# Kernel optimization log

Hardware: AMD Instinct MI355X
Metric: run time of the kernel (lower is better)

## Reference

```python
import jax, jax.numpy as jnp
import numpy as np

V, E, H, B, T = 32000, 256, 512, 64, 24

def setup_inputs() -> dict:
    key = jax.random.key(0)
    ks = jax.random.split(key, 24)
    def n(k, shape, s=0.02):
        return jax.random.normal(k, shape, dtype=jnp.float32) * s
    inp = {
        "question_feat": n(ks[0], (B, H), 1.0),
        "image_feat": n(ks[1], (B, H), 1.0),
        "answer_seq": jax.random.randint(ks[2], (B, T), 0, V),
        "embedding": n(ks[3], (V, E)),
        "attn_W": n(ks[4], (H, 3 * H)),
        "attn_b": jnp.zeros((H,), jnp.float32),
        "v_W": n(ks[5], (1, H)),
        "fc_W": n(ks[6], (V, H)),
        "fc_b": jnp.zeros((V,), jnp.float32),
    }
    in_sizes = [E + 2 * H, H, H]  # layer0 sees cat(embed, context)=1280
    for l in range(3):
        inp[f"W_ih{l}"] = n(ks[7 + 4 * l], (4 * H, in_sizes[l]))
        inp[f"W_hh{l}"] = n(ks[8 + 4 * l], (4 * H, H))
        inp[f"b_ih{l}"] = jnp.zeros((4 * H,), jnp.float32)
        inp[f"b_hh{l}"] = jnp.zeros((4 * H,), jnp.float32)
    return inp

def _lstm_cell(x, h, c, W_ih, W_hh, b_ih, b_hh):
    # torch gate order: i, f, g, o
    g = x @ W_ih.T + b_ih + h @ W_hh.T + b_hh
    i, f, gg, o = jnp.split(g, 4, axis=-1)
    c_new = jax.nn.sigmoid(f) * c + jax.nn.sigmoid(i) * jnp.tanh(gg)
    h_new = jax.nn.sigmoid(o) * jnp.tanh(c_new)
    return h_new, c_new

def reference(question_feat, image_feat, answer_seq, embedding, attn_W, attn_b, v_W,
              fc_W, fc_b,
              W_ih0, W_hh0, b_ih0, b_hh0,
              W_ih1, W_hh1, b_ih1, b_hh1,
              W_ih2, W_hh2, b_ih2, b_hh2):
    combined = jnp.concatenate([question_feat, image_feat], axis=1)  # [B, 2H]
    x = embedding[answer_seq]            # [B, T, E]
    xs = jnp.swapaxes(x, 0, 1)           # [T, B, E]
    Ws = ((W_ih0, W_hh0, b_ih0, b_hh0),
          (W_ih1, W_hh1, b_ih1, b_hh1),
          (W_ih2, W_hh2, b_ih2, b_hh2))

    def step(carry, x_t):
        h, c, prev_attn = carry          # h, c: [3, B, H]; prev_attn: [B, H]
        energy = jnp.tanh(jnp.concatenate([prev_attn, combined], axis=1) @ attn_W.T + attn_b)
        aw = jax.nn.softmax(energy @ v_W.T, axis=1)  # [B, 1] (softmax over singleton, faithful to source)
        ctx = aw * combined                          # [B, 2H]
        cur = jnp.concatenate([x_t, ctx], axis=1)    # [B, E+2H]
        hs, cs = [], []
        for l in range(3):
            nh, nc = _lstm_cell(cur, h[l], c[l], *Ws[l])
            hs.append(nh); cs.append(nc); cur = nh
        logits = cur @ fc_W.T + fc_b                 # [B, V]
        return (jnp.stack(hs), jnp.stack(cs), cur), logits

    hdim = question_feat.shape[1]
    bsz = question_feat.shape[0]
    h0 = jnp.zeros((3, bsz, hdim), question_feat.dtype)
    c0 = jnp.zeros((3, bsz, hdim), question_feat.dtype)
    _, outs = jax.lax.scan(step, (h0, c0, question_feat), xs)
    return jnp.swapaxes(outs, 0, 1)  # [B, T, V]
```

## Files before the change

### kernel.cpp

```cpp
#include <hip/hip_runtime.h>
#include <hip/hip_bf16.h>
#include <stdint.h>


typedef short bf16x8 __attribute__((ext_vector_type(8)));
typedef float f32x4 __attribute__((ext_vector_type(4)));

#define NLSTM 96
#define FCB   160
#define NTILE_N 250
#define HSLOT 32768

__device__ __forceinline__ unsigned short f2b(float f) {
    uint32_t u = __builtin_bit_cast(uint32_t, f);
    uint32_t r = u + 0x7FFFu + ((u >> 16) & 1u);
    return (unsigned short)(r >> 16);
}
__device__ __forceinline__ float fsig(float x) {
    float e = __expf(-x);
    return __builtin_amdgcn_rcpf(1.0f + e);
}
__device__ __forceinline__ float ftanh(float x) {
    float e = __expf(-2.0f * x);
    return (1.0f - e) * __builtin_amdgcn_rcpf(1.0f + e);
}

__global__ __launch_bounds__(128) void pack_w(
    const float* __restrict__ Whh0,
    const float* __restrict__ Wih1, const float* __restrict__ Whh1,
    const float* __restrict__ Wih2, const float* __restrict__ Whh2,
    unsigned short* __restrict__ Wpk)
{
    int gid = blockIdx.x;
    int layer = gid / (32 * 64);
    int rem = gid % (32 * 64);
    int lbid = rem >> 6, r = rem & 63;
    int q = r >> 4, jj = r & 15;
    int grow = q * 512 + lbid * 16 + jj;
    int K = (layer == 0) ? 512 : 1024;
    size_t wbase = (layer == 0) ? 0
                 : (layer == 1) ? (size_t)32 * 64 * 512
                                : (size_t)32 * 64 * 512 + (size_t)32 * 64 * 1024;
    unsigned short* dst = Wpk + wbase + ((size_t)lbid * 64 + r) * K;
    const float *s0, *s1 = nullptr;
    if (layer == 0)      { s0 = Whh0 + (size_t)grow * 512; }
    else if (layer == 1) { s0 = Wih1 + (size_t)grow * 512; s1 = Whh1 + (size_t)grow * 512; }
    else                 { s0 = Wih2 + (size_t)grow * 512; s1 = Whh2 + (size_t)grow * 512; }
    {
        int k4 = threadIdx.x;
        f32x4 v = *(const f32x4*)&s0[k4 * 4];
        unsigned short o[4];
        #pragma unroll
        for (int j = 0; j < 4; ++j) o[j] = f2b(v[j]);
        *(uint64_t*)&dst[k4 * 4] = *(uint64_t*)o;
    }
    if (s1) {
        int k4 = threadIdx.x;
        f32x4 v = *(const f32x4*)&s1[k4 * 4];
        unsigned short o[4];
        #pragma unroll
        for (int j = 0; j < 4; ++j) o[j] = f2b(v[j]);
        *(uint64_t*)&dst[512 + k4 * 4] = *(uint64_t*)o;
    }
}

__global__ __launch_bounds__(256) void build_x(
    const float* __restrict__ qf,
    const float* __restrict__ imf,
    const int* __restrict__ seq,
    const float* __restrict__ emb,
    unsigned short* __restrict__ X)
{
    int r = blockIdx.x;
    int t = r >> 6, b = r & 63;
    int tok = seq[b * 24 + t];
    for (int e = threadIdx.x; e < 1280; e += 256) {
        float v;
        if (e < 256)      v = emb[(size_t)tok * 256 + e];
        else if (e < 768) v = qf[b * 512 + (e - 256)];
        else              v = imf[b * 512 + (e - 768)];
        X[(size_t)r * 1280 + e] = f2b(v);
    }
}

__global__ __launch_bounds__(256) void gemm128(
    const unsigned short* __restrict__ A, int lda,
    const float* __restrict__ Wf, int ldb,
    int K,
    const float* __restrict__ bias0,
    const float* __restrict__ bias1,
    float* __restrict__ outf, int ldo, int mblocks, int xcdq)
{
    __shared__ unsigned short lA[128 * 72];
    __shared__ unsigned short lB[128 * 72];
    int lin = blockIdx.x;
    int wg = (lin & 7) * xcdq + (lin >> 3);
    const int m0 = (wg % mblocks) * 128, n0 = (wg / mblocks) * 128;
    const int tid = threadIdx.x;
    const int lane = tid & 63, wid = tid >> 6;
    const int wm = wid >> 1, wn = wid & 1;

    f32x4 acc[4][4] = {};

    for (int kt = 0; kt < K; kt += 64) {
        #pragma unroll
        for (int c = 0; c < 4; ++c) {
            int chunk = tid + c * 256;
            int row = chunk >> 3, kc = (chunk & 7) * 8;
            *(bf16x8*)&lA[row * 72 + kc] =
                *(const bf16x8*)&A[(size_t)(m0 + row) * lda + kt + kc];
            const float* bp = &Wf[(size_t)(n0 + row) * ldb + kt + kc];
            f32x4 v0 = *(const f32x4*)bp;
            f32x4 v1 = *(const f32x4*)(bp + 4);
            unsigned short o[8];
            #pragma unroll
            for (int x = 0; x < 4; ++x) { o[x] = f2b(v0[x]); o[4 + x] = f2b(v1[x]); }
            *(bf16x8*)&lB[row * 72 + kc] = *(bf16x8*)o;
        }
        __syncthreads();
        #pragma unroll
        for (int ks = 0; ks < 64; ks += 32) {
            int kl = ks + ((lane >> 4) << 3);
            bf16x8 af[4], bfr[4];
            #pragma unroll
            for (int i = 0; i < 4; ++i)
                af[i] = *(const bf16x8*)&lA[(wm * 64 + i * 16 + (lane & 15)) * 72 + kl];
            #pragma unroll
            for (int j = 0; j < 4; ++j)
                bfr[j] = *(const bf16x8*)&lB[(wn * 64 + j * 16 + (lane & 15)) * 72 + kl];
            #pragma unroll
            for (int i = 0; i < 4; ++i)
                #pragma unroll
                for (int j = 0; j < 4; ++j)
                    acc[i][j] = __builtin_amdgcn_mfma_f32_16x16x32_bf16(
                        af[i], bfr[j], acc[i][j], 0, 0, 0);
        }
        __syncthreads();
    }

    #pragma unroll
    for (int i = 0; i < 4; ++i) {
        #pragma unroll
        for (int j = 0; j < 4; ++j) {
            int n = n0 + wn * 64 + j * 16 + (lane & 15);
            float bias = bias0[n] + bias1[n];
            #pragma unroll
            for (int r = 0; r < 4; ++r) {
                int m = m0 + wm * 64 + i * 16 + ((lane >> 4) << 2) + r;
                outf[(size_t)m * ldo + n] = acc[i][j][r] + bias;
            }
        }
    }
}

#define ISSUE_CHUNK(buf, kb0)                                                 \
    {                                                                         \
        _Pragma("unroll")                                                     \
        for (int u_ = 0; u_ < 8; ++u_) {                                      \
            int kg_ = (kb0) + u_ * 32 + lk;                                   \
            const unsigned short* hb_ = (kg_ < 512) ? A0 : A1;                \
            int kk_ = kg_ & 511;                                              \
            const unsigned short* ap_ =                                       \
                hb_ + ((kk_ >> 4) << 10) + brow16 + (kk_ & 15);               \
            asm volatile("global_load_dwordx4 %0, %1, off sc1"                \
                         : "=v"(buf[u_]) : "v"(ap_) : "memory");              \
        }                                                                     \
    }
#define MFMA_CHUNK(buf, kb0)                                                  \
    {                                                                         \
        _Pragma("unroll")                                                     \
        for (int u_ = 0; u_ < 8; ++u_) {                                      \
            int ksl_ = (kb0) + u_ * 32 + lk;                                  \
            _Pragma("unroll")                                                 \
            for (int q_ = 0; q_ < 4; ++q_) {                                  \
                int gx_ = ((ksl_ >> 3) ^ (lrow & 7)) << 3;                    \
                bf16x8 bq_ = *(const bf16x8*)&lb[(q_ * 16 + lrow) * K + gx_]; \
                acc[q_] = __builtin_amdgcn_mfma_f32_16x16x32_bf16(            \
                    buf[u_], bq_, acc[q_], 0, 0, 0);                          \
            }                                                                 \
        }                                                                     \
    }
#define VM_WAIT(n) { asm volatile("s_waitcnt vmcnt(" #n ")" ::: "memory");    \
                     __builtin_amdgcn_sched_barrier(0); }

#define FC_ISSUE_G(buf, ks0)                                                  \
    {                                                                         \
        _Pragma("unroll")                                                     \
        for (int u_ = 0; u_ < 4; ++u_) {                                      \
            _Pragma("unroll")                                                 \
            for (int i_ = 0; i_ < 4; ++i_) {                                  \
                int rm_ = m0 + wm * 64 + i_ * 16 + lrow;                      \
                int k_ = (ks0) + u_ * 32 + lk;                                \
                const unsigned short* ap_ = h2                                \
                    + (size_t)((rm_ >> 6) + 1) * HSLOT                        \
                    + ((k_ >> 4) << 10) + ((rm_ & 63) << 4) + (k_ & 15);      \
                asm volatile("global_load_dwordx4 %0, %1, off sc1"            \
                             : "=v"(buf[u_ * 4 + i_]) : "v"(ap_) : "memory"); \
            }                                                                 \
        }                                                                     \
    }
#define FC_MFMA_G(buf, ks0)                                                   \
    {                                                                         \
        _Pragma("unroll")                                                     \
        for (int u_ = 0; u_ < 4; ++u_) {                                      \
            int ks_ = (ks0) + u_ * 32 + lk;                                   \
            _Pragma("unroll")                                                 \
            for (int jj_ = 0; jj_ < 4; ++jj_) {                               \
                int row_ = wn * 64 + jj_ * 16 + lrow;                         \
                int gx_ = ((ks_ >> 3) ^ (row_ & 7)) << 3;                     \
                bf16x8 bq_ = *(const bf16x8*)&lB[row_ * 512 + gx_];           \
                _Pragma("unroll")                                             \
                for (int i_ = 0; i_ < 4; ++i_)                                \
                    acc[i_][jj_] = __builtin_amdgcn_mfma_f32_16x16x32_bf16(   \
                        buf[u_ * 4 + i_], bq_, acc[i_][jj_], 0, 0, 0);        \
            }                                                                 \
        }                                                                     \
    }

__global__ __launch_bounds__(256, 1) void fused_wave(
    const unsigned short* __restrict__ Wpk,
    const float* __restrict__ G0,
    const float* __restrict__ bih1, const float* __restrict__ bhh1,
    const float* __restrict__ bih2, const float* __restrict__ bhh2,
    unsigned short* __restrict__ hst,
    unsigned int* __restrict__ flags,
    const float* __restrict__ fcW,
    const float* __restrict__ fcb,
    float* __restrict__ out)
{
    extern __shared__ char smem[];
    const int bid = blockIdx.x;
    const int tid = threadIdx.x;
    const int lane = tid & 63, w = tid >> 6;
    const int lrow = lane & 15, lk = (lane >> 4) * 8;

    if (bid < NLSTM) {
        unsigned short* lb = (unsigned short*)smem;
        unsigned int* lcnt = (unsigned int*)(smem + 131072);
        const int layer = bid >> 5;
        const int lbid = bid & 31;
        const int j0 = lbid * 16;

        const int K = (layer == 0) ? 512 : 1024;
        const size_t wbase = (layer == 0) ? 0
                           : (layer == 1) ? (size_t)32 * 64 * 512
                                          : (size_t)32 * 64 * 512 + (size_t)32 * 64 * 1024;
        const unsigned short* Wblk = Wpk + wbase + (size_t)lbid * 64 * K;

        if (tid < 24) lcnt[tid] = 0;
        {
            const int kshift = (layer == 0) ? 6 : 7;
            const int gm = (K >> 3) - 1;
            const int total = 64 << kshift;
            for (int idx = tid; idx < total; idx += 256) {
                int row = idx >> kshift, g = idx & gm;
                int gx = g ^ (row & 7);
                *(bf16x8*)&lb[row * K + gx * 8] =
                    *(const bf16x8*)&Wblk[(size_t)row * K + g * 8];
            }
        }
        __syncthreads();

        unsigned short* hl = hst + (size_t)layer * 25 * HSLOT;
        const unsigned short* hlow =
            (layer > 0) ? hst + (size_t)(layer - 1) * 25 * HSLOT : nullptr;

        float pb[4] = {0.f, 0.f, 0.f, 0.f};
        if (layer == 1) {
            #pragma unroll
            for (int q = 0; q < 4; ++q)
                pb[q] = bih1[q * 512 + j0 + lrow] + bhh1[q * 512 + j0 + lrow];
        } else if (layer == 2) {
            #pragma unroll
            for (int q = 0; q < 4; ++q)
                pb[q] = bih2[q * 512 + j0 + lrow] + bhh2[q * 512 + j0 + lrow];
        }

        float creg[4] = {0.f, 0.f, 0.f, 0.f};
        const int brow16 = (w * 16 + lrow) << 4;

        for (int t = 0; t < 24; ++t) {
            float g0p[16];
            if (layer == 0) {
                const float* gp = G0 + (size_t)t * 64 * 2048;
                #pragma unroll
                for (int r = 0; r < 4; ++r) {
                    int b = w * 16 + ((lane >> 4) << 2) + r;
                    #pragma unroll
                    for (int q = 0; q < 4; ++q)
                        g0p[r * 4 + q] = gp[(size_t)b * 2048 + q * 512 + j0 + lrow];
                }
            }
            if (layer > 0 || t > 0) {
                const unsigned int* f1;
                const unsigned int* f2 = nullptr;
                if (layer == 0) {
                    f1 = flags + (t - 1) * 32;
                } else {
                    f1 = flags + ((layer - 1) * 24 + t) * 32;
                    if (t > 0) f2 = flags + (layer * 24 + t - 1) * 32;
                }
                const unsigned int* fp = (lane < 32) ? f1 : (f2 ? f2 : f1);
                int idx = lane & 31;
                while (true) {
                    unsigned v = __hip_atomic_load((unsigned int*)&fp[idx],
                                                   __ATOMIC_RELAXED,
                                                   __HIP_MEMORY_SCOPE_AGENT);
                    if (__all(v != 0)) break;
                    __builtin_amdgcn_s_sleep(2);
                }
            }

            const unsigned short* A0 = (layer == 0)
                ? hl + (size_t)t * HSLOT
                : hlow + (size_t)(t + 1) * HSLOT;
            const unsigned short* A1 = (layer == 0)
                ? A0
                : hl + (size_t)t * HSLOT;

            f32x4 acc[4] = {};
            bf16x8 bufA[8], bufB[8], bufC[8], bufD[8];
            if (K == 1024) {
                ISSUE_CHUNK(bufA, 0); ISSUE_CHUNK(bufB, 256);
                ISSUE_CHUNK(bufC, 512); ISSUE_CHUNK(bufD, 768);
                VM_WAIT(24); MFMA_CHUNK(bufA, 0);
                VM_WAIT(16); MFMA_CHUNK(bufB, 256);
                VM_WAIT(8);  MFMA_CHUNK(bufC, 512);
                VM_WAIT(0);  MFMA_CHUNK(bufD, 768);
            } else {
                ISSUE_CHUNK(bufA, 0); ISSUE_CHUNK(bufB, 256);
                VM_WAIT(8); MFMA_CHUNK(bufA, 0);
                VM_WAIT(0); MFMA_CHUNK(bufB, 256);
            }

            unsigned short* hslot = hl + (size_t)(t + 1) * HSLOT + (lbid << 10);
            #pragma unroll
            for (int r = 0; r < 4; ++r) {
                int b = w * 16 + ((lane >> 4) << 2) + r;
                float g[4];
                #pragma unroll
                for (int q = 0; q < 4; ++q) {
                    float p = (layer == 0) ? g0p[r * 4 + q] : pb[q];
                    g[q] = acc[q][r] + p;
                }
                float ig = fsig(g[0]);
                float fg = fsig(g[1]);
                float gg = ftanh(g[2]);
                float og = fsig(g[3]);
                float cn = fg * creg[r] + ig * gg;
                creg[r] = cn;
                float h = og * ftanh(cn);
                unsigned int hb = (unsigned int)f2b(h);
                unsigned short* hp = hslot + (b << 4) + lrow;
                asm volatile("global_store_short %0, %1, off sc1"
                             :: "v"(hp), "v"(hb) : "memory");
            }
            asm volatile("s_waitcnt vmcnt(0)" ::: "memory");
            if (lane == 0) {
                unsigned old = atomicAdd(&lcnt[t], 1u);
                if (old == 3u)
                    __hip_atomic_store(&flags[(layer * 24 + t) * 32 + lbid], 1u,
                                       __ATOMIC_RELAXED, __HIP_MEMORY_SCOPE_AGENT);
            }
        }
    } else {
        unsigned short* lB = (unsigned short*)smem;
        const int f = bid - NLSTM;
        const int wm = w >> 1, wn = w & 1;
        const unsigned short* h2 = hst + (size_t)2 * 25 * HSLOT;

        for (int p = 0; p < 2; ++p) {
            int ntp = f + p * FCB;
            if (ntp >= NTILE_N) break;
            int n0 = ntp * 128;
            __syncthreads();
            for (int idx = tid; idx < 128 * 64; idx += 256) {
                int row = idx >> 6, g = idx & 63;
                const float* bp = &fcW[(size_t)(n0 + row) * 512 + g * 8];
                f32x4 v0 = *(const f32x4*)bp;
                f32x4 v1 = *(const f32x4*)(bp + 4);
                unsigned short o[8];
                #pragma unroll
                for (int x = 0; x < 4; ++x) { o[x] = f2b(v0[x]); o[4 + x] = f2b(v1[x]); }
                *(bf16x8*)&lB[row * 512 + ((g ^ (row & 7)) << 3)] = *(bf16x8*)o;
            }
            __syncthreads();

            for (int mt = 0; mt < 12; ++mt) {
                if (tid < 64) {
                    const unsigned int* fb = flags + (2 * 24 + 2 * mt) * 32;
                    while (true) {
                        unsigned v = __hip_atomic_load((unsigned int*)&fb[lane],
                                                       __ATOMIC_RELAXED,
                                                       __HIP_MEMORY_SCOPE_AGENT);
                        if (__all(v != 0)) break;
                        __builtin_amdgcn_s_sleep(32);
                    }
                }
                __syncthreads();

                int m0 = mt * 128;
                f32x4 acc[4][4] = {};
                bf16x8 gA[16], gB[16];
                FC_ISSUE_G(gA, 0); FC_ISSUE_G(gB, 128);
                VM_WAIT(16); FC_MFMA_G(gA, 0);
                FC_ISSUE_G(gA, 256);
                VM_WAIT(16); FC_MFMA_G(gB, 128);
                FC_ISSUE_G(gB, 384);
                VM_WAIT(16); FC_MFMA_G(gA, 256);
                VM_WAIT(0);  FC_MFMA_G(gB, 384);

                #pragma unroll
                for (int i = 0; i < 4; ++i) {
                    #pragma unroll
                    for (int jj = 0; jj < 4; ++jj) {
                        int n = n0 + wn * 64 + jj * 16 + lrow;
                        float bias = fcb[n];
                        #pragma unroll
                        for (int r = 0; r < 4; ++r) {
                            int m = m0 + wm * 64 + i * 16 + ((lane >> 4) << 2) + r;
                            int b = m & 63, t = m >> 6;
                            __builtin_nontemporal_store(
                                acc[i][jj][r] + bias,
                                &out[(size_t)(b * 24 + t) * 32000 + n]);
                        }
                    }
                }
            }
        }
    }
}

extern "C" void kernel_launch(void* const* d_in, const int* in_sizes, int n_in,
                              void* d_out, int out_size, void* d_ws, size_t ws_size,
                              hipStream_t stream) {
    const float* qf  = (const float*)d_in[0];
    const float* imf = (const float*)d_in[1];
    const int*   seq = (const int*)d_in[2];
    const float* emb = (const float*)d_in[3];
    const float* fcW = (const float*)d_in[7];
    const float* fcb = (const float*)d_in[8];
    const float* Wih[3] = {(const float*)d_in[9],  (const float*)d_in[13], (const float*)d_in[17]};
    const float* Whh[3] = {(const float*)d_in[10], (const float*)d_in[14], (const float*)d_in[18]};
    const float* bih[3] = {(const float*)d_in[11], (const float*)d_in[15], (const float*)d_in[19]};
    const float* bhh[3] = {(const float*)d_in[12], (const float*)d_in[16], (const float*)d_in[20]};

    char* ws = (char*)d_ws;
    unsigned short* X     = (unsigned short*)(ws + 0);
    float*          G0    = (float*)(ws + 3932160);
    unsigned short* hst   = (unsigned short*)(ws + 16515072);
    unsigned int*   flags = (unsigned int*)(ws + 21430272);
    unsigned short* Wpk   = (unsigned short*)(ws + 21440000);

    hipMemsetAsync(flags, 0, 9216, stream);
    for (int l = 0; l < 3; ++l)
        hipMemsetAsync(hst + (size_t)l * 25 * HSLOT, 0, HSLOT * 2, stream);

    pack_w<<<3 * 32 * 64, 128, 0, stream>>>(Whh[0], Wih[1], Whh[1], Wih[2], Whh[2], Wpk);
    build_x<<<1536, 256, 0, stream>>>(qf, imf, seq, emb, X);

    gemm128<<<192, 256, 0, stream>>>(
        X, 1280, Wih[0], 1280, 1280, bih[0], bhh[0], G0, 2048, 12, 192 / 8);

    fused_wave<<<NLSTM + FCB, 256, 131200, stream>>>(
        Wpk, G0, bih[1], bhh[1], bih[2], bhh[2], hst, flags,
        fcW, fcb, (float*)d_out);
}
```

Measured before the change: 317.0 us.

## Use per-wave completion flags and stage FC A-tiles through LDS

LSTM blocks no longer count completed waves with an LDS atomic before setting one flag per block. Each wave now sets its own flag, and consumers poll four times as many flags, which removes the intra-block counter serialization. The FC blocks now load the h-state A tiles into a 16 KB LDS buffer with global_load_lds in 8 k-chunks, then do MFMA from LDS. This replaces the direct global-to-register double-buffered loads. The change adds more syncthreads, drops the register-level load/compute overlap, and enlarges the flag area and the LDS allocation.

```diff
diff --git a/kernel.cpp b/kernel.cpp
--- a/kernel.cpp
+++ b/kernel.cpp
@@ -23,6 +23,11 @@
 __device__ __forceinline__ float ftanh(float x) {
     float e = __expf(-2.0f * x);
     return (1.0f - e) * __builtin_amdgcn_rcpf(1.0f + e);
+}
+__device__ __forceinline__ void gload_lds16(const unsigned short* g, unsigned short* l) {
+    __builtin_amdgcn_global_load_lds(
+        (const __attribute__((address_space(1))) unsigned int*)g,
+        (__attribute__((address_space(3))) unsigned int*)l, 16, 0, 16);
 }
 
 __global__ __launch_bounds__(128) void pack_w(
@@ -183,40 +188,6 @@
 #define VM_WAIT(n) { asm volatile("s_waitcnt vmcnt(" #n ")" ::: "memory");    \
                      __builtin_amdgcn_sched_barrier(0); }
 
-#define FC_ISSUE_G(buf, ks0)                                                  \
-    {                                                                         \
-        _Pragma("unroll")                                                     \
-        for (int u_ = 0; u_ < 4; ++u_) {                                      \
-            _Pragma("unroll")                                                 \
-            for (int i_ = 0; i_ < 4; ++i_) {                                  \
-                int rm_ = m0 + wm * 64 + i_ * 16 + lrow;                      \
-                int k_ = (ks0) + u_ * 32 + lk;                                \
-                const unsigned short* ap_ = h2                                \
-                    + (size_t)((rm_ >> 6) + 1) * HSLOT                        \
-                    + ((k_ >> 4) << 10) + ((rm_ & 63) << 4) + (k_ & 15);      \
-                asm volatile("global_load_dwordx4 %0, %1, off sc1"            \
-                             : "=v"(buf[u_ * 4 + i_]) : "v"(ap_) : "memory"); \
-            }                                                                 \
-        }                                                                     \
-    }
-#define FC_MFMA_G(buf, ks0)                                                   \
-    {                                                                         \
-        _Pragma("unroll")                                                     \
-        for (int u_ = 0; u_ < 4; ++u_) {                                      \
-            int ks_ = (ks0) + u_ * 32 + lk;                                   \
-            _Pragma("unroll")                                                 \
-            for (int jj_ = 0; jj_ < 4; ++jj_) {                               \
-                int row_ = wn * 64 + jj_ * 16 + lrow;                         \
-                int gx_ = ((ks_ >> 3) ^ (row_ & 7)) << 3;                     \
-                bf16x8 bq_ = *(const bf16x8*)&lB[row_ * 512 + gx_];           \
-                _Pragma("unroll")                                             \
-                for (int i_ = 0; i_ < 4; ++i_)                                \
-                    acc[i_][jj_] = __builtin_amdgcn_mfma_f32_16x16x32_bf16(   \
-                        buf[u_ * 4 + i_], bq_, acc[i_][jj_], 0, 0, 0);        \
-            }                                                                 \
-        }                                                                     \
-    }
-
 __global__ __launch_bounds__(256, 1) void fused_wave(
     const unsigned short* __restrict__ Wpk,
     const float* __restrict__ G0,
@@ -236,7 +207,6 @@
 
     if (bid < NLSTM) {
         unsigned short* lb = (unsigned short*)smem;
-        unsigned int* lcnt = (unsigned int*)(smem + 131072);
         const int layer = bid >> 5;
         const int lbid = bid & 31;
         const int j0 = lbid * 16;
@@ -247,7 +217,6 @@
                                           : (size_t)32 * 64 * 512 + (size_t)32 * 64 * 1024;
         const unsigned short* Wblk = Wpk + wbase + (size_t)lbid * 64 * K;
 
-        if (tid < 24) lcnt[tid] = 0;
         {
             const int kshift = (layer == 0) ? 6 : 7;
             const int gm = (K >> 3) - 1;
@@ -295,18 +264,24 @@
                 const unsigned int* f1;
                 const unsigned int* f2 = nullptr;
                 if (layer == 0) {
-                    f1 = flags + (t - 1) * 32;
+                    f1 = flags + (t - 1) * 128;
                 } else {
-                    f1 = flags + ((layer - 1) * 24 + t) * 32;
-                    if (t > 0) f2 = flags + (layer * 24 + t - 1) * 32;
-                }
-                const unsigned int* fp = (lane < 32) ? f1 : (f2 ? f2 : f1);
-                int idx = lane & 31;
+                    f1 = flags + ((layer - 1) * 24 + t) * 128;
+                    if (t > 0) f2 = flags + (layer * 24 + t - 1) * 128;
+                }
                 while (true) {
-                    unsigned v = __hip_atomic_load((unsigned int*)&fp[idx],
-                                                   __ATOMIC_RELAXED,
-                                                   __HIP_MEMORY_SCOPE_AGENT);
-                    if (__all(v != 0)) break;
+                    unsigned ok =
+                        (__hip_atomic_load((unsigned int*)&f1[lane], __ATOMIC_RELAXED,
+                                           __HIP_MEMORY_SCOPE_AGENT) != 0u) &
+                        (__hip_atomic_load((unsigned int*)&f1[64 + lane], __ATOMIC_RELAXED,
+                                           __HIP_MEMORY_SCOPE_AGENT) != 0u);
+                    if (f2) {
+                        ok &= (__hip_atomic_load((unsigned int*)&f2[lane], __ATOMIC_RELAXED,
+                                                 __HIP_MEMORY_SCOPE_AGENT) != 0u) &
+                              (__hip_atomic_load((unsigned int*)&f2[64 + lane], __ATOMIC_RELAXED,
+                                                 __HIP_MEMORY_SCOPE_AGENT) != 0u);
+                    }
+                    if (__all(ok)) break;
                     __builtin_amdgcn_s_sleep(2);
                 }
             }
@@ -357,14 +332,13 @@
             }
             asm volatile("s_waitcnt vmcnt(0)" ::: "memory");
             if (lane == 0) {
-                unsigned old = atomicAdd(&lcnt[t], 1u);
-                if (old == 3u)
-                    __hip_atomic_store(&flags[(layer * 24 + t) * 32 + lbid], 1u,
-                                       __ATOMIC_RELAXED, __HIP_MEMORY_SCOPE_AGENT);
+                __hip_atomic_store(&flags[(layer * 24 + t) * 128 + lbid * 4 + w], 1u,
+                                   __ATOMIC_RELAXED, __HIP_MEMORY_SCOPE_AGENT);
             }
         }
     } else {
         unsigned short* lB = (unsigned short*)smem;
+        unsigned short* lA16 = (unsigned short*)(smem + 131072);
         const int f = bid - NLSTM;
         const int wm = w >> 1, wn = w & 1;
         const unsigned short* h2 = hst + (size_t)2 * 25 * HSLOT;
@@ -388,27 +362,61 @@
 
             for (int mt = 0; mt < 12; ++mt) {
                 if (tid < 64) {
-                    const unsigned int* fb = flags + (2 * 24 + 2 * mt) * 32;
+                    const unsigned int* fb = flags + (2 * 24 + 2 * mt) * 128;
                     while (true) {
-                        unsigned v = __hip_atomic_load((unsigned int*)&fb[lane],
-                                                       __ATOMIC_RELAXED,
-                                                       __HIP_MEMORY_SCOPE_AGENT);
-                        if (__all(v != 0)) break;
-                        __builtin_amdgcn_s_sleep(32);
+                        unsigned ok = 1u;
+                        #pragma unroll
+                        for (int s = 0; s < 4; ++s)
+                            ok &= (__hip_atomic_load((unsigned int*)&fb[s * 64 + lane],
+                                                     __ATOMIC_RELAXED,
+                                                     __HIP_MEMORY_SCOPE_AGENT) != 0u);
+                        if (__all(ok)) break;
+                        __builtin_amdgcn_s_sleep(16);
                     }
                 }
                 __syncthreads();
 
                 int m0 = mt * 128;
                 f32x4 acc[4][4] = {};
-                bf16x8 gA[16], gB[16];
-                FC_ISSUE_G(gA, 0); FC_ISSUE_G(gB, 128);
-                VM_WAIT(16); FC_MFMA_G(gA, 0);
-                FC_ISSUE_G(gA, 256);
-                VM_WAIT(16); FC_MFMA_G(gB, 128);
-                FC_ISSUE_G(gB, 384);
-                VM_WAIT(16); FC_MFMA_G(gA, 256);
-                VM_WAIT(0);  FC_MFMA_G(gB, 384);
+                for (int c = 0; c < 8; ++c) {
+                    #pragma unroll
+                    for (int ps = 0; ps < 4; ++ps) {
+                        int oe = ps * 2048 + tid * 8;
+                        int ts = oe >> 12;
+                        int e = oe & 4095;
+                        int slab = e >> 10;
+                        int row = (e >> 4) & 63;
+                        int colh = e & 15;
+                        const unsigned short* g = h2
+                            + (size_t)(2 * mt + ts + 1) * HSLOT
+                            + ((4 * c + slab) << 10) + (row << 4) + colh;
+                        gload_lds16(g, &lA16[oe]);
+                    }
+                    VM_WAIT(0);
+                    __syncthreads();
+                    #pragma unroll
+                    for (int kt2 = 0; kt2 < 2; ++kt2) {
+                        bf16x8 af[4];
+                        #pragma unroll
+                        for (int i = 0; i < 4; ++i) {
+                            int oe = wm * 4096 + (((kt2 * 32 + lk) >> 4) << 10)
+                                   + ((i * 16 + lrow) << 4) + (lk & 8);
+                            af[i] = *(const bf16x8*)&lA16[oe];
+                        }
+                        #pragma unroll
+                        for (int jj = 0; jj < 4; ++jj) {
+                            int row_ = wn * 64 + jj * 16 + lrow;
+                            int ks_ = c * 64 + kt2 * 32 + lk;
+                            int gx_ = ((ks_ >> 3) ^ (row_ & 7)) << 3;
+                            bf16x8 bq = *(const bf16x8*)&lB[row_ * 512 + gx_];
+                            #pragma unroll
+                            for (int i = 0; i < 4; ++i)
+                                acc[i][jj] = __builtin_amdgcn_mfma_f32_16x16x32_bf16(
+                                    af[i], bq, acc[i][jj], 0, 0, 0);
+                        }
+                    }
+                    __syncthreads();
+                }
 
                 #pragma unroll
                 for (int i = 0; i < 4; ++i) {
@@ -450,9 +458,9 @@
     float*          G0    = (float*)(ws + 3932160);
     unsigned short* hst   = (unsigned short*)(ws + 16515072);
     unsigned int*   flags = (unsigned int*)(ws + 21430272);
-    unsigned short* Wpk   = (unsigned short*)(ws + 21440000);
-
-    hipMemsetAsync(flags, 0, 9216, stream);
+    unsigned short* Wpk   = (unsigned short*)(ws + 21467136);
+
+    hipMemsetAsync(flags, 0, 36864, stream);
     for (int l = 0; l < 3; ++l)
         hipMemsetAsync(hst + (size_t)l * 25 * HSLOT, 0, HSLOT * 2, stream);
 
@@ -462,7 +470,7 @@
     gemm128<<<192, 256, 0, stream>>>(
         X, 1280, Wih[0], 1280, 1280, bih[0], bhh[0], G0, 2048, 12, 192 / 8);
 
-    fused_wave<<<NLSTM + FCB, 256, 131200, stream>>>(
+    fused_wave<<<NLSTM + FCB, 256, 147456, stream>>>(
         Wpk, G0, bih[1], bhh[1], bih[2], bhh[2], hst, flags,
         fcW, fcb, (float*)d_out);
 }
```

After: 345.3 us. 1.09x slower.
